# Kernel optimization log

Hardware: AMD Instinct MI355X
Metric: run time of the kernel (lower is better)

Reference implementation:

```python
import jax, jax.numpy as jnp
import numpy as np

N = 100000; C = 128; H = 8; G = C // 4
B = 2; Z = 40; Y = 996; X = 996
WIN = 12; NUM_WIN = 200; EPS = 1e-3


def _make_indices():
    rng = np.random.RandomState(0)
    total = B * Z * Y * X
    uk = np.unique(rng.randint(0, total, size=300000).astype(np.int64))[:N]
    b = uk // (Z * Y * X); r = uk % (Z * Y * X)
    z = r // (Y * X); r = r % (Y * X)
    y = r // X; x = r % X
    return b, z, y, x, uk


def _neighbors(b, z, y, x, keys, offsets):
    # submanifold conv: output only at active sites; lookup coord+offset in active set
    sk = np.sort(keys); order = np.argsort(keys)
    cols = []
    for dz, dy, dx in offsets:
        nz, ny, nx = z + dz, y + dy, x + dx
        valid = (nz >= 0) & (nz < Z) & (ny >= 0) & (ny < Y) & (nx >= 0) & (nx < X)
        cand = ((b * Z + nz) * Y + ny) * X + nx
        pos = np.searchsorted(sk, cand)
        posc = np.minimum(pos, N - 1)
        found = valid & (sk[posc] == cand)
        cols.append(np.where(found, order[posc], N))  # N = sentinel (zero row)
    return np.stack(cols, axis=1).astype(np.int32)


def setup_inputs() -> dict:
    b, z, y, x, keys = _make_indices()
    off_k = [(dz, dy, dx) for dz in (-1, 0, 1) for dy in (-1, 0, 1) for dx in (-1, 0, 1)]
    off_h = [(0, 0, d) for d in range(-6, 7)]  # kernel (1,1,13) along x
    off_w = [(0, d, 0) for d in range(-6, 7)]  # kernel (1,13,1) along y
    nbr_k = _neighbors(b, z, y, x, keys, off_k)
    nbr_h = _neighbors(b, z, y, x, keys, off_h)
    nbr_w = _neighbors(b, z, y, x, keys, off_w)
    coords = np.stack([y, x], axis=0)
    wis = []
    for d in range(2):
        wkey = b * 1000 + coords[d] // WIN
        _, inv = np.unique(wkey, return_inverse=True)
        wis.append(inv)
    win_inds = np.stack(wis, 0).astype(np.int32)

    ks = jax.random.split(jax.random.key(0), 20)
    s = 0.05
    return dict(
        feats=jax.random.normal(ks[0], (N, C), jnp.float32),
        win_inds=jnp.asarray(win_inds),
        nbr_k=jnp.asarray(nbr_k), nbr_h=jnp.asarray(nbr_h), nbr_w=jnp.asarray(nbr_w),
        bn_g=jnp.ones((2, C)) + s * jax.random.normal(ks[1], (2, C)),
        bn_b=s * jax.random.normal(ks[2], (2, C)),
        Wqkv=s * jax.random.normal(ks[3], (2, C, 3 * C)),
        Wproj=s * jax.random.normal(ks[4], (2, C, C)),
        bproj=s * jax.random.normal(ks[5], (2, C)),
        bn1_g=jnp.ones((2, C)) + s * jax.random.normal(ks[6], (2, C)),
        bn1_b=s * jax.random.normal(ks[7], (2, C)),
        Wk=s * jax.random.normal(ks[8], (2, 27, G, G)),
        Wh=s * jax.random.normal(ks[9], (2, 13, G, G)),
        Ww=s * jax.random.normal(ks[10], (2, 13, G, G)),
        bn2_g=jnp.ones((2, C)) + s * jax.random.normal(ks[11], (2, C)),
        bn2_b=s * jax.random.normal(ks[12], (2, C)),
        fc1_W=s * jax.random.normal(ks[13], (2, C, 2 * C)),
        fc1_b=s * jax.random.normal(ks[14], (2, 2 * C)),
        fc2_W=s * jax.random.normal(ks[15], (2, 2 * C, C)),
        fc2_b=s * jax.random.normal(ks[16], (2, C)),
    )


def _bn(x, g, b):
    # BatchNorm1d, training-mode batch statistics, eps=1e-3
    m = jnp.mean(x, 0)
    v = jnp.var(x, 0)
    return (x - m) * jax.lax.rsqrt(v + EPS) * g + b


def _attn(x, wi, Wqkv, Wp, bp):
    # windowed linear attention: per-window K^T V + normalization by sum(K)
    q, k, v = jnp.split(x @ Wqkv, 3, axis=1)
    q = jax.nn.relu(q).reshape(N, H, C // H)
    k = jax.nn.relu(k).reshape(N, H, C // H)
    v = v.reshape(N, H, C // H)
    kv = jax.ops.segment_sum(jnp.einsum('nhc,nhd->nhcd', k, v), wi, NUM_WIN)
    s = jax.ops.segment_sum(k, wi, NUM_WIN)
    y = jnp.einsum('nhc,nhcd->nhd', q, kv[wi])
    z = jnp.sum(s[wi] * q, -1, keepdims=True)
    y = (y / (z + EPS)).reshape(N, C)
    return y @ Wp + bp


def _subm(f, nbr, W):
    # submanifold sparse conv via precomputed neighbor map (sentinel row = zeros)
    fp = jnp.concatenate([f, jnp.zeros((1, f.shape[1]), f.dtype)], 0)
    return jnp.einsum('nkc,kcd->nd', fp[nbr], W)


def reference(feats, win_inds, nbr_k, nbr_h, nbr_w, bn_g, bn_b, Wqkv, Wproj, bproj,
              bn1_g, bn1_b, Wk, Wh, Ww, bn2_g, bn2_b, fc1_W, fc1_b, fc2_W, fc2_b):
    f = feats
    for d in range(2):  # directions
        x = _attn(_bn(f, bn_g[d], bn_b[d]), win_inds[d], Wqkv[d], Wproj[d], bproj[d])
        f = f + x
        # CWI_FFN_Layer_3D
        fb = _bn(f, bn1_g[d], bn1_b[d])
        f2 = jnp.concatenate([
            _subm(fb[:, :G], nbr_k, Wk[d]),
            _subm(fb[:, G:2 * G], nbr_h, Wh[d]),
            _subm(fb[:, 2 * G:3 * G], nbr_w, Ww[d]),
            fb[:, 3 * G:],
        ], axis=1)
        f = fb + f2
        h = _bn(f, bn2_g[d], bn2_b[d])
        f = f + (jax.nn.relu(h @ fc1_W[d] + fc1_b[d]) @ fc2_W[d] + fc2_b[d])
    return f
```

## Files before the change

### kernel.cpp

```cpp
#include <hip/hip_runtime.h>
#include <math.h>

#define NPTS 100000
#define CCH 128
#define NWIN 200
#define NBLK_STATS 512
#define NBLK_SORT 391
#define SEGSZ 128
#define NSEG_MAX 1024

#define BM 128
#define BN 128
#define BK 64

typedef __attribute__((ext_vector_type(8))) short bf16x8;
typedef __attribute__((ext_vector_type(4))) float f32x4;
typedef __attribute__((ext_vector_type(4))) unsigned short u16x4;

__device__ __forceinline__ unsigned short f2bf(float f) {
    union { float f; unsigned u; } x; x.f = f;
    unsigned r = x.u + 0x7fff + ((x.u >> 16) & 1);
    return (unsigned short)(r >> 16);
}
__device__ __forceinline__ float bf2f(unsigned short h) {
    union { unsigned u; float f; } x; x.u = ((unsigned)h) << 16;
    return x.f;
}

__global__ __launch_bounds__(256) void bn_partial(const float* __restrict__ F,
                                                  float* __restrict__ part) {
    int t = threadIdx.x;
    int b = blockIdx.x;
    int rg = t >> 5;
    int c4 = (t & 31) * 4;
    float s0=0.f,s1=0.f,s2=0.f,s3=0.f,q0=0.f,q1=0.f,q2=0.f,q3=0.f;
    for (int n = b * 8 + rg; n < NPTS; n += NBLK_STATS * 8) {
        float4 v = *reinterpret_cast<const float4*>(&F[(size_t)n * CCH + c4]);
        s0 += v.x; s1 += v.y; s2 += v.z; s3 += v.w;
        q0 += v.x*v.x; q1 += v.y*v.y; q2 += v.z*v.z; q3 += v.w*v.w;
    }
    __shared__ float red[8][256];
    red[rg][c4+0] = s0; red[rg][c4+1] = s1; red[rg][c4+2] = s2; red[rg][c4+3] = s3;
    red[rg][128+c4+0] = q0; red[rg][128+c4+1] = q1; red[rg][128+c4+2] = q2; red[rg][128+c4+3] = q3;
    __syncthreads();
    float a = 0.f;
#pragma unroll
    for (int g = 0; g < 8; g++) a += red[g][t];
    part[b * 256 + t] = a;
}

__global__ __launch_bounds__(256) void bnred_k(const float* __restrict__ part,
                                               float* __restrict__ part2) {
    int t = threadIdx.x;
    int i = blockIdx.x;
    float a = 0.f;
#pragma unroll 8
    for (int j = 0; j < 32; j++) a += part[(size_t)(i * 32 + j) * 256 + t];
    part2[i * 256 + t] = a;
}

__global__ void bn_finalize(const float* __restrict__ part2,
                            const float* __restrict__ g, const float* __restrict__ bb,
                            float* __restrict__ scale, float* __restrict__ shift) {
    int c = threadIdx.x;
    double s = 0.0, q = 0.0;
#pragma unroll
    for (int b = 0; b < 16; b++) {
        s += (double)part2[b * 256 + c];
        q += (double)part2[b * 256 + 128 + c];
    }
    double m = s / (double)NPTS;
    double var = q / (double)NPTS - m * m;
    double rstd = 1.0 / sqrt(var + 1e-3);
    float sc = (float)rstd * g[c];
    scale[c] = sc;
    shift[c] = bb[c] - (float)m * sc;
}

__global__ __launch_bounds__(128) void wprep(
    const float* __restrict__ W, int K, int N,
    const float* __restrict__ sc, const float* __restrict__ sh,
    const float* __restrict__ bias,
    unsigned short* __restrict__ WT, float* __restrict__ biasf)
{
    int n = blockIdx.x;
    int t = threadIdx.x;
    float part = 0.f;
    for (int k = t; k < K; k += 128) {
        float w = W[(size_t)k * N + n];
        float s = sc ? sc[k] * w : w;
        WT[(size_t)n * K + k] = f2bf(s);
        if (sh) part += sh[k] * w;
    }
    __shared__ float red[128];
    red[t] = part;
    __syncthreads();
    for (int o = 64; o > 0; o >>= 1) {
        if (t < o) red[t] += red[t + o];
        __syncthreads();
    }
    if (t == 0) biasf[n] = red[0] + (bias ? bias[n] : 0.f);
}

__global__ void wconv_prep_all(const float* __restrict__ Wk, const float* __restrict__ Wh,
                               const float* __restrict__ Ww, unsigned short* __restrict__ WB) {
    int i = blockIdx.x * 256 + threadIdx.x;
    if (i >= 53 * 1024) return;
    int tap = i >> 10; int rem = i & 1023; int dd = rem >> 5; int c = rem & 31;
    const float* src; int lt;
    if (tap < 27)      { src = Wk; lt = tap; }
    else if (tap < 40) { src = Wh; lt = tap - 27; }
    else               { src = Ww; lt = tap - 40; }
    WB[i] = f2bf(src[lt * 1024 + c * 32 + dd]);
}

template<int NT>
__global__ __launch_bounds__(256) void gemm_knt(
    const float* __restrict__ A, int lda,
    const unsigned short* __restrict__ WT, const float* __restrict__ biasf,
    unsigned short* __restrict__ Out, int ldo, int reluLim)
{
    __shared__ __align__(16) char smem[49664];
    unsigned short* As = (unsigned short*)smem;
    unsigned short* Bs = (unsigned short*)(smem + 32768);
    float* Ep = (float*)(smem + 32768);

    const int tid  = threadIdx.x;
    const int wave = tid >> 6;
    const int lane = tid & 63;
    const int bm = blockIdx.x * BM;
    const int lrow = lane & 15;
    const int lhk  = lane >> 4;

#pragma unroll
    for (int pass = 0; pass < 16; pass++) {
        int row = pass * 8 + (tid >> 5);
        int grow = bm + row;
        int c4 = (tid & 31) * 4;
        float4 v = make_float4(0.f, 0.f, 0.f, 0.f);
        if (grow < NPTS)
            v = *reinterpret_cast<const float4*>(&A[(size_t)grow * lda + c4]);
        u16x4 h4 = { f2bf(v.x), f2bf(v.y), f2bf(v.z), f2bf(v.w) };
        int half = c4 >> 6;
        int cw = c4 & 63;
        int sw = (cw >> 3) ^ (row & 7);
        *reinterpret_cast<u16x4*>(&As[row * 128 + half * 64 + sw * 8 + (cw & 7)]) = h4;
    }

    for (int nt = 0; nt < NT; nt++) {
        const int bn = nt * BN;
        f32x4 acc[2][8];
#pragma unroll
        for (int i = 0; i < 2; i++)
#pragma unroll
            for (int j = 0; j < 8; j++)
                acc[i][j] = (f32x4){0.f, 0.f, 0.f, 0.f};

#pragma unroll
        for (int h = 0; h < 2; h++) {
            __syncthreads();
#pragma unroll
            for (int pass = 0; pass < 4; pass++) {
                int n = pass * 32 + (tid >> 3);
                bf16x8 w = *reinterpret_cast<const bf16x8*>(
                    &WT[(size_t)(bn + n) * 128 + h * 64 + (tid & 7) * 8]);
                int sw = (tid & 7) ^ (n & 7);
                *reinterpret_cast<bf16x8*>(&Bs[n * 64 + sw * 8]) = w;
            }
            __syncthreads();
#pragma unroll
            for (int ks = 0; ks < 2; ks++) {
                bf16x8 af[2], bfr[8];
#pragma unroll
                for (int fi = 0; fi < 2; fi++) {
                    int row = wave * 32 + fi * 16 + lrow;
                    int sw = (ks * 4 + lhk) ^ (row & 7);
                    af[fi] = *reinterpret_cast<const bf16x8*>(&As[row * 128 + h * 64 + sw * 8]);
                }
#pragma unroll
                for (int fj = 0; fj < 8; fj++) {
                    int col = fj * 16 + lrow;
                    int sw = (ks * 4 + lhk) ^ (col & 7);
                    bfr[fj] = *reinterpret_cast<const bf16x8*>(&Bs[col * 64 + sw * 8]);
                }
#pragma unroll
                for (int fi = 0; fi < 2; fi++)
#pragma unroll
                    for (int fj = 0; fj < 8; fj++)
                        acc[fi][fj] = __builtin_amdgcn_mfma_f32_16x16x32_bf16(
                            af[fi], bfr[fj], acc[fi][fj], 0, 0, 0);
            }
        }
        __syncthreads();

#pragma unroll
        for (int ch = 0; ch < 4; ch++) {
            if (wave == ch) {
#pragma unroll
                for (int fi = 0; fi < 2; fi++)
#pragma unroll
                    for (int fj = 0; fj < 8; fj++) {
                        int r0 = fi * 16 + lhk * 4;
                        int col = fj * 16 + lrow;
#pragma unroll
                        for (int r = 0; r < 4; r++)
                            Ep[(r0 + r) * 132 + col] = acc[fi][fj][r];
                    }
            }
            __syncthreads();
#pragma unroll
            for (int pass = 0; pass < 4; pass++) {
                int idx = pass * 256 + tid;
                int r = idx >> 5;
                int c4 = (idx & 31) * 4;
                int rr = bm + ch * 32 + r;
                if (rr < NPTS) {
                    float4 v = *reinterpret_cast<const float4*>(&Ep[r * 132 + c4]);
                    float4 b = *reinterpret_cast<const float4*>(&biasf[bn + c4]);
                    v.x += b.x; v.y += b.y; v.z += b.z; v.w += b.w;
                    int col = bn + c4;
                    if (col + 0 < reluLim) v.x = fmaxf(v.x, 0.f);
                    if (col + 1 < reluLim) v.y = fmaxf(v.y, 0.f);
                    if (col + 2 < reluLim) v.z = fmaxf(v.z, 0.f);
                    if (col + 3 < reluLim) v.w = fmaxf(v.w, 0.f);
                    u16x4 hv = { f2bf(v.x), f2bf(v.y), f2bf(v.z), f2bf(v.w) };
                    *reinterpret_cast<u16x4*>(&Out[(size_t)rr * ldo + bn + c4]) = hv;
                }
            }
            __syncthreads();
        }
    }
}

template<int ABF, int OBF>
__global__ __launch_bounds__(256) void gemm_t(
    const void* __restrict__ Ap, int lda,
    const unsigned short* __restrict__ WT, const float* __restrict__ biasf,
    int K,
    void* __restrict__ Outp, int ldo,
    int reluLim, int addFlag)
{
    __shared__ __align__(16) char smem[34048];
    unsigned short* As = (unsigned short*)smem;
    unsigned short* Bs = As + BM * BK;
    float* Ep = (float*)smem;

    const int tid  = threadIdx.x;
    const int wave = tid >> 6;
    const int lane = tid & 63;
    const int bm = blockIdx.y * BM;
    const int bn = blockIdx.x * BN;

    f32x4 acc[2][8];
#pragma unroll
    for (int i = 0; i < 2; i++)
#pragma unroll
        for (int j = 0; j < 8; j++)
            acc[i][j] = (f32x4){0.f, 0.f, 0.f, 0.f};

    const int lrow = lane & 15;
    const int lhk  = lane >> 4;

    for (int kk = 0; kk < K; kk += BK) {
        if (ABF) {
            const unsigned short* Ab = (const unsigned short*)Ap;
#pragma unroll
            for (int pass = 0; pass < 4; pass++) {
                int row = pass * 32 + (tid >> 3);
                int grow = bm + row;
                bf16x8 w = (bf16x8){0,0,0,0,0,0,0,0};
                if (grow < NPTS)
                    w = *reinterpret_cast<const bf16x8*>(&Ab[(size_t)grow * lda + kk + (tid & 7) * 8]);
                int sw = (tid & 7) ^ (row & 7);
                *reinterpret_cast<bf16x8*>(&As[row * 64 + sw * 8]) = w;
            }
        } else {
            const float* Af = (const float*)Ap;
            const int arow_t = tid >> 4;
            const int acol   = (tid & 15) * 4;
#pragma unroll
            for (int pass = 0; pass < 8; pass++) {
                int row = pass * 16 + arow_t;
                int grow = bm + row;
                float4 v = make_float4(0.f, 0.f, 0.f, 0.f);
                if (grow < NPTS)
                    v = *reinterpret_cast<const float4*>(&Af[(size_t)grow * lda + kk + acol]);
                u16x4 h = { f2bf(v.x), f2bf(v.y), f2bf(v.z), f2bf(v.w) };
                int s = acol >> 3;
                int sw = s ^ (row & 7);
                *reinterpret_cast<u16x4*>(&As[row * 64 + sw * 8 + (acol & 7)]) = h;
            }
        }
#pragma unroll
        for (int pass = 0; pass < 4; pass++) {
            int n = pass * 32 + (tid >> 3);
            bf16x8 w = *reinterpret_cast<const bf16x8*>(&WT[(size_t)(bn + n) * K + kk + (tid & 7) * 8]);
            int sw = (tid & 7) ^ (n & 7);
            *reinterpret_cast<bf16x8*>(&Bs[n * 64 + sw * 8]) = w;
        }
        __syncthreads();

#pragma unroll
        for (int ks = 0; ks < 2; ks++) {
            bf16x8 af[2], bfr[8];
#pragma unroll
            for (int fi = 0; fi < 2; fi++) {
                int row = wave * 32 + fi * 16 + lrow;
                int sw = (ks * 4 + lhk) ^ (row & 7);
                af[fi] = *reinterpret_cast<const bf16x8*>(&As[row * 64 + sw * 8]);
            }
#pragma unroll
            for (int fj = 0; fj < 8; fj++) {
                int col = fj * 16 + lrow;
                int sw = (ks * 4 + lhk) ^ (col & 7);
                bfr[fj] = *reinterpret_cast<const bf16x8*>(&Bs[col * 64 + sw * 8]);
            }
#pragma unroll
            for (int fi = 0; fi < 2; fi++)
#pragma unroll
                for (int fj = 0; fj < 8; fj++)
                    acc[fi][fj] = __builtin_amdgcn_mfma_f32_16x16x32_bf16(
                        af[fi], bfr[fj], acc[fi][fj], 0, 0, 0);
        }
        __syncthreads();
    }

    for (int hh = 0; hh < 2; hh++) {
        if ((wave >> 1) == hh) {
#pragma unroll
            for (int fi = 0; fi < 2; fi++) {
                int row = (wave & 1) * 32 + fi * 16 + (lane >> 4) * 4;
#pragma unroll
                for (int fj = 0; fj < 8; fj++) {
                    int col = fj * 16 + (lane & 15);
#pragma unroll
                    for (int r = 0; r < 4; r++)
                        Ep[(row + r) * 132 + col] = acc[fi][fj][r];
                }
            }
        }
        __syncthreads();
#pragma unroll
        for (int pass = 0; pass < 8; pass++) {
            int idx = pass * 256 + tid;
            int r = idx >> 5;
            int c4 = (idx & 31) * 4;
            int rr = bm + hh * 64 + r;
            if (rr < NPTS) {
                float4 v = *reinterpret_cast<const float4*>(&Ep[r * 132 + c4]);
                float4 b = *reinterpret_cast<const float4*>(&biasf[bn + c4]);
                v.x += b.x; v.y += b.y; v.z += b.z; v.w += b.w;
                int col = bn + c4;
                if (col + 0 < reluLim) v.x = fmaxf(v.x, 0.f);
                if (col + 1 < reluLim) v.y = fmaxf(v.y, 0.f);
                if (col + 2 < reluLim) v.z = fmaxf(v.z, 0.f);
                if (col + 3 < reluLim) v.w = fmaxf(v.w, 0.f);
                if (OBF) {
                    unsigned short* o = (unsigned short*)Outp + (size_t)rr * ldo + bn + c4;
                    u16x4 hv = { f2bf(v.x), f2bf(v.y), f2bf(v.z), f2bf(v.w) };
                    *reinterpret_cast<u16x4*>(o) = hv;
                } else {
                    float* o = (float*)Outp + (size_t)rr * ldo + bn + c4;
                    if (addFlag) {
                        float4 ov = *reinterpret_cast<const float4*>(o);
                        v.x += ov.x; v.y += ov.y; v.z += ov.z; v.w += ov.w;
                    }
                    *reinterpret_cast<float4*>(o) = v;
                }
            }
        }
        __syncthreads();
    }
}

__global__ __launch_bounds__(256) void hist2_k(const int* __restrict__ wi,
                                               int* __restrict__ BH) {
    __shared__ int h[NWIN];
    int t = threadIdx.x;
    if (t < NWIN) h[t] = 0;
    __syncthreads();
    int n = blockIdx.x * 256 + t;
    if (n < NPTS) atomicAdd(&h[wi[n]], 1);
    __syncthreads();
    if (t < NWIN) BH[blockIdx.x * 256 + t] = h[t];
}

__global__ __launch_bounds__(256) void colscan2_k(const int* __restrict__ BH,
                                                  int* __restrict__ OFFB,
                                                  int* __restrict__ TOT) {
    int w = blockIdx.x;
    int t = threadIdx.x;
    __shared__ int s[512];
    int v0 = (t < NBLK_SORT) ? BH[t * 256 + w] : 0;
    int v1 = (t + 256 < NBLK_SORT) ? BH[(t + 256) * 256 + w] : 0;
    s[t] = v0; s[t + 256] = v1;
    __syncthreads();
#pragma unroll
    for (int off = 1; off < 512; off <<= 1) {
        int a0 = (t >= off) ? s[t - off] : 0;
        int a1 = (t + 256 >= off) ? s[t + 256 - off] : 0;
        __syncthreads();
        s[t] += a0;
        s[t + 256] += a1;
        __syncthreads();
    }
    if (t < NBLK_SORT) OFFB[t * 256 + w] = s[t] - v0;
    if (t + 256 < NBLK_SORT) OFFB[(t + 256) * 256 + w] = s[t + 256] - v1;
    if (t == 0) TOT[w] = s[NBLK_SORT - 1];
}

__global__ __launch_bounds__(256) void meta2_k(const int* __restrict__ TOT,
                                               int* __restrict__ OFFS,
                                               int* __restrict__ SEGW, int* __restrict__ SEGP0,
                                               int* __restrict__ SEGP1, int* __restrict__ SEGBASE) {
    __shared__ int offs[NWIN + 1];
    __shared__ int segc[NWIN];
    int t = threadIdx.x;
    if (t < NWIN) segc[t] = TOT[t];
    __syncthreads();
    if (t == 0) {
        int a = 0;
        for (int w = 0; w < NWIN; w++) { int c = segc[w]; offs[w] = a; a += c; }
        offs[NWIN] = a;
    }
    __syncthreads();
    if (t <= NWIN) OFFS[t] = offs[t];
    if (t < NWIN) segc[t] = (offs[t + 1] - offs[t] + SEGSZ - 1) / SEGSZ;
    __syncthreads();
    if (t == 0) {
        int a = 0;
        for (int i = 0; i < NWIN; i++) { int c = segc[i]; segc[i] = a; SEGBASE[i] = a; a += c; }
        SEGBASE[NWIN] = a;
    }
    __syncthreads();
    if (t < NWIN) {
        int b = segc[t];
        int p0 = offs[t], p1 = offs[t + 1];
        for (int p = p0; p < p1; p += SEGSZ) {
            SEGW[b] = t; SEGP0[b] = p; SEGP1[b] = min(p + SEGSZ, p1); b++;
        }
    }
}

__global__ __launch_bounds__(256) void scatter2_k(const int* __restrict__ wi,
                                                  const int* __restrict__ OFFS,
                                                  const int* __restrict__ OFFB,
                                                  int* __restrict__ list) {
    __shared__ int h[NWIN];
    int t = threadIdx.x;
    if (t < NWIN) h[t] = 0;
    __syncthreads();
    int n = blockIdx.x * 256 + t;
    if (n < NPTS) {
        int w = wi[n];
        int r = atomicAdd(&h[w], 1);
        list[OFFS[w] + OFFB[blockIdx.x * 256 + w] + r] = n;
    }
}

__global__ __launch_bounds__(256) void window_kv_seg(
    const unsigned short* __restrict__ R0bf,
    const int* __restrict__ list,
    const int* __restrict__ SEGP0, const int* __restrict__ SEGP1,
    const int* __restrict__ SEGBASE,
    float* __restrict__ PKV)
{
    int sid = blockIdx.x;
    if (sid >= SEGBASE[NWIN]) return;
    int t = threadIdx.x;
    int p0 = SEGP0[sid], p1 = SEGP1[sid];
    __shared__ float buf[8][256];
    float acc[8] = {0.f,0.f,0.f,0.f,0.f,0.f,0.f,0.f};
    float sa = 0.f;
    int f0 = t * 8;
    int h = f0 >> 8;
    int c = (f0 >> 4) & 15;
    int d0 = f0 & 15;
    const int sr = t >> 5;
    const int c8 = (t & 31) * 8;

    for (int g = p0; g < p1; g += 8) {
        int m = min(8, p1 - g);
        int nj[8];
#pragma unroll
        for (int j = 0; j < 8; j++)
            nj[j] = list[(g + j < p1) ? g + j : p1 - 1];
        __syncthreads();
        {
            const unsigned short* row = &R0bf[(size_t)nj[sr] * 384 + 128];
            bf16x8 hv = *reinterpret_cast<const bf16x8*>(&row[c8]);
            float4 lo = make_float4(bf2f((unsigned short)hv[0]), bf2f((unsigned short)hv[1]),
                                    bf2f((unsigned short)hv[2]), bf2f((unsigned short)hv[3]));
            float4 hi = make_float4(bf2f((unsigned short)hv[4]), bf2f((unsigned short)hv[5]),
                                    bf2f((unsigned short)hv[6]), bf2f((unsigned short)hv[7]));
            *reinterpret_cast<float4*>(&buf[sr][c8]) = lo;
            *reinterpret_cast<float4*>(&buf[sr][c8 + 4]) = hi;
        }
        __syncthreads();
#pragma unroll
        for (int j = 0; j < 8; j++) {
            if (j >= m) break;
            float kc = buf[j][h * 16 + c];
#pragma unroll
            for (int i = 0; i < 8; i++) acc[i] += kc * buf[j][128 + h * 16 + d0 + i];
            if (t < 128) sa += buf[j][t];
        }
    }
    float* out = &PKV[(size_t)sid * 2176];
#pragma unroll
    for (int i = 0; i < 8; i++) out[f0 + i] = acc[i];
    if (t < 128) out[2048 + t] = sa;
}

__global__ __launch_bounds__(256) void kv_reduce(
    const float* __restrict__ PKV, const int* __restrict__ SEGBASE,
    float* __restrict__ KV, float* __restrict__ SB)
{
    int w = blockIdx.x;
    int t = threadIdx.x;
    int s0 = SEGBASE[w], s1 = SEGBASE[w + 1];
    float a[8] = {0.f,0.f,0.f,0.f,0.f,0.f,0.f,0.f};
    float sb = 0.f;
    for (int s = s0; s < s1; s++) {
        const float* p = &PKV[(size_t)s * 2176];
#pragma unroll
        for (int i = 0; i < 8; i++) a[i] += p[t * 8 + i];
        if (t < 128) sb += p[2048 + t];
    }
#pragma unroll
    for (int i = 0; i < 8; i++) KV[w * 2048 + t * 8 + i] = a[i];
    if (t < 128) SB[w * 128 + t] = sb;
}

__global__ __launch_bounds__(256) void attn_y_seg(
    const unsigned short* __restrict__ R0bf,
    unsigned short* __restrict__ Ybf,
    const int* __restrict__ list,
    const int* __restrict__ SEGW, const int* __restrict__ SEGP0,
    const int* __restrict__ SEGP1, const int* __restrict__ SEGBASE,
    const float* __restrict__ KV, const float* __restrict__ SB)
{
    int sid = blockIdx.x;
    if (sid >= SEGBASE[NWIN]) return;
    int t = threadIdx.x;
    int w = SEGW[sid];
    int g  = t >> 5;
    int h  = (t >> 2) & 7;
    int d4 = (t & 3) * 4;

    float4 kvr[16];
    const float* kvb = &KV[w * 2048 + h * 256 + d4];
#pragma unroll
    for (int cc = 0; cc < 16; cc++)
        kvr[cc] = *reinterpret_cast<const float4*>(&kvb[cc * 16]);
    float sreg[16];
    const float* sb = &SB[w * 128 + h * 16];
#pragma unroll
    for (int cc = 0; cc < 16; cc++) sreg[cc] = sb[cc];

    int p0 = SEGP0[sid], p1 = SEGP1[sid];
    for (int p = p0 + g; p < p1; p += 8) {
        int n = list[p];
        const unsigned short* q = &R0bf[(size_t)n * 384 + h * 16];
        bf16x8 qa = *reinterpret_cast<const bf16x8*>(&q[0]);
        bf16x8 qb = *reinterpret_cast<const bf16x8*>(&q[8]);
        float qq[16];
#pragma unroll
        for (int i = 0; i < 8; i++) {
            qq[i] = bf2f((unsigned short)qa[i]);
            qq[8 + i] = bf2f((unsigned short)qb[i]);
        }
        float z = 0.f;
        float4 y = make_float4(0.f, 0.f, 0.f, 0.f);
#pragma unroll
        for (int cc = 0; cc < 16; cc++) {
            z += qq[cc] * sreg[cc];
            y.x += qq[cc] * kvr[cc].x;
            y.y += qq[cc] * kvr[cc].y;
            y.z += qq[cc] * kvr[cc].z;
            y.w += qq[cc] * kvr[cc].w;
        }
        float inv = 1.f / (z + 1e-3f);
        u16x4 o = { f2bf(y.x * inv), f2bf(y.y * inv), f2bf(y.z * inv), f2bf(y.w * inv) };
        *reinterpret_cast<u16x4*>(&Ybf[(size_t)n * 128 + h * 16 + d4]) = o;
    }
}

__global__ void bn_apply(float* F, unsigned short* __restrict__ FBbf,
                         const float* __restrict__ scale, const float* __restrict__ shift)
{
    int i = blockIdx.x * 256 + threadIdx.x;
    int n = i >> 5;
    int c4 = (i & 31) * 4;
    float4 v = *reinterpret_cast<const float4*>(&F[n * CCH + c4]);
    float4 o;
    o.x = v.x * scale[c4 + 0] + shift[c4 + 0];
    o.y = v.y * scale[c4 + 1] + shift[c4 + 1];
    o.z = v.z * scale[c4 + 2] + shift[c4 + 2];
    o.w = v.w * scale[c4 + 3] + shift[c4 + 3];
    u16x4 hv = { f2bf(o.x), f2bf(o.y), f2bf(o.z), f2bf(o.w) };
    *reinterpret_cast<u16x4*>(&FBbf[(size_t)n * 128 + c4]) = hv;
    if (c4 >= 96) {
        float4 t = make_float4(2.f * o.x, 2.f * o.y, 2.f * o.z, 2.f * o.w);
        *reinterpret_cast<float4*>(&F[n * CCH + c4]) = t;
    }
}

template<int KN>
__global__ __launch_bounds__(256) void conv_direct(
    const int* __restrict__ nbrA, const int* __restrict__ nbrB,
    const unsigned short* __restrict__ WBall, int wbBase,
    const unsigned short* __restrict__ FBbf,
    float* __restrict__ F, int offBase)
{
    const int which = blockIdx.y;
    const int* __restrict__ nbr = which ? nbrB : nbrA;
    const int off = offBase + which * 32;
    const unsigned short* __restrict__ WB = WBall + wbBase + which * KN * 1024;

    __shared__ __align__(16) float Ep[128 * 36];

    const int tid = threadIdx.x;
    const int wave = tid >> 6;
    const int lane = tid & 63;
    const int bm = blockIdx.x * 128;
    const int lrow = lane & 15;
    const int lk = lane >> 4;

    const int row0 = bm + wave * 32 + lrow;
    const int row1 = row0 + 16;

    f32x4 acc[2][2];
#pragma unroll
    for (int i = 0; i < 2; i++)
#pragma unroll
        for (int j = 0; j < 2; j++)
            acc[i][j] = (f32x4){0.f, 0.f, 0.f, 0.f};

    constexpr int CHK = (KN == 27) ? 9 : 13;
    for (int c0 = 0; c0 < KN; c0 += CHK) {
        int i0[CHK], i1[CHK];
#pragma unroll
        for (int j = 0; j < CHK; j++) {
            i0[j] = (row0 < NPTS) ? nbr[(size_t)row0 * KN + c0 + j] : NPTS;
            i1[j] = (row1 < NPTS) ? nbr[(size_t)row1 * KN + c0 + j] : NPTS;
        }
#pragma unroll
        for (int j = 0; j < CHK; j++) {
            int k = c0 + j;
            bf16x8 a0 = (bf16x8){0,0,0,0,0,0,0,0};
            bf16x8 a1 = (bf16x8){0,0,0,0,0,0,0,0};
            if (i0[j] < NPTS)
                a0 = *reinterpret_cast<const bf16x8*>(&FBbf[(size_t)i0[j] * 128 + off + lk * 8]);
            if (i1[j] < NPTS)
                a1 = *reinterpret_cast<const bf16x8*>(&FBbf[(size_t)i1[j] * 128 + off + lk * 8]);
            bf16x8 b0 = *reinterpret_cast<const bf16x8*>(&WB[k * 1024 + lrow * 32 + lk * 8]);
            bf16x8 b1 = *reinterpret_cast<const bf16x8*>(&WB[k * 1024 + (16 + lrow) * 32 + lk * 8]);
            acc[0][0] = __builtin_amdgcn_mfma_f32_16x16x32_bf16(a0, b0, acc[0][0], 0, 0, 0);
            acc[0][1] = __builtin_amdgcn_mfma_f32_16x16x32_bf16(a0, b1, acc[0][1], 0, 0, 0);
            acc[1][0] = __builtin_amdgcn_mfma_f32_16x16x32_bf16(a1, b0, acc[1][0], 0, 0, 0);
            acc[1][1] = __builtin_amdgcn_mfma_f32_16x16x32_bf16(a1, b1, acc[1][1], 0, 0, 0);
        }
    }

#pragma unroll
    for (int fi = 0; fi < 2; fi++)
#pragma unroll
        for (int fj = 0; fj < 2; fj++) {
            int r0 = wave * 32 + fi * 16 + lk * 4;
            int col = fj * 16 + lrow;
#pragma unroll
            for (int r = 0; r < 4; r++)
                Ep[(r0 + r) * 36 + col] = acc[fi][fj][r];
        }
    __syncthreads();
#pragma unroll
    for (int pass = 0; pass < 4; pass++) {
        int idx = pass * 256 + tid;
        int r = idx >> 3;
        int c4 = (idx & 7) * 4;
        int rr = bm + r;
        if (rr < NPTS) {
            float4 v = *reinterpret_cast<const float4*>(&Ep[r * 36 + c4]);
            u16x4 fbh = *reinterpret_cast<const u16x4*>(&FBbf[(size_t)rr * 128 + off + c4]);
            v.x += bf2f(fbh.x); v.y += bf2f(fbh.y);
            v.z += bf2f(fbh.z); v.w += bf2f(fbh.w);
            *reinterpret_cast<float4*>(&F[(size_t)rr * CCH + off + c4]) = v;
        }
    }
}

extern "C" void kernel_launch(void* const* d_in, const int* in_sizes, int n_in,
                              void* d_out, int out_size, void* d_ws, size_t ws_size,
                              hipStream_t stream)
{
    const float* feats   = (const float*)d_in[0];
    const int*   win_inds= (const int*)d_in[1];
    const int*   nbr_k   = (const int*)d_in[2];
    const int*   nbr_h   = (const int*)d_in[3];
    const int*   nbr_w   = (const int*)d_in[4];
    const float* bn_g    = (const float*)d_in[5];
    const float* bn_b    = (const float*)d_in[6];
    const float* Wqkv    = (const float*)d_in[7];
    const float* Wproj   = (const float*)d_in[8];
    const float* bproj   = (const float*)d_in[9];
    const float* bn1_g   = (const float*)d_in[10];
    const float* bn1_b   = (const float*)d_in[11];
    const float* Wk      = (const float*)d_in[12];
    const float* Wh      = (const float*)d_in[13];
    const float* Ww      = (const float*)d_in[14];
    const float* bn2_g   = (const float*)d_in[15];
    const float* bn2_b   = (const float*)d_in[16];
    const float* fc1_W   = (const float*)d_in[17];
    const float* fc1_b   = (const float*)d_in[18];
    const float* fc2_W   = (const float*)d_in[19];
    const float* fc2_b   = (const float*)d_in[20];

    float* F  = (float*)d_out;
    float* KV = (float*)d_ws;
    float* SB = KV + NWIN * 2048;
    float* ST = SB + NWIN * 128;
    float* PART = ST + 768;
    float* PART2 = PART + NBLK_STATS * 256;
    float* PKV = PART2 + 16 * 256;
    int* OFFS = (int*)(PKV + (size_t)NSEG_MAX * 2176);
    int* TOT  = OFFS + 256;
    int* LIST = TOT + 256;
    int* BH   = LIST + 100096;
    int* OFFB = BH + NBLK_SORT * 256;
    int* SEGW = OFFB + NBLK_SORT * 256;
    int* SEGP0= SEGW + NSEG_MAX;
    int* SEGP1= SEGP0 + NSEG_MAX;
    int* SEGBASE = SEGP1 + NSEG_MAX;
    unsigned short* WQKVT = (unsigned short*)(SEGBASE + 256);
    unsigned short* WPROJT = WQKVT + 384 * 128;
    unsigned short* WFC1T  = WPROJT + 128 * 128;
    unsigned short* WFC2T  = WFC1T + 256 * 128;
    float* BQKV  = (float*)(WFC2T + 128 * 256);
    float* BPROJ = BQKV + 384;
    float* BFC1  = BPROJ + 128;
    float* BFC2  = BFC1 + 256;
    unsigned short* R0bf = (unsigned short*)(BFC2 + 128);
    unsigned short* Hbf  = R0bf;
    unsigned short* Ybf  = R0bf + (size_t)NPTS * 384;
    unsigned short* FBbf = Ybf + (size_t)NPTS * 128;
    unsigned short* WBall= FBbf + (size_t)NPTS * 128;

    hipMemcpyAsync(F, feats, (size_t)NPTS * CCH * sizeof(float),
                   hipMemcpyDeviceToDevice, stream);

    dim3 g1(1, 782);
    dim3 gc13(782, 2);

    for (int d = 0; d < 2; d++) {
        const int* wi = win_inds + (size_t)d * NPTS;
        float* SC0 = ST, *SH0 = ST + 128, *SC1 = ST + 256, *SH1 = ST + 384,
             * SC2 = ST + 512, *SH2 = ST + 640;

        bn_partial<<<NBLK_STATS, 256, 0, stream>>>(F, PART);
        bnred_k<<<16, 256, 0, stream>>>(PART, PART2);
        bn_finalize<<<1, 128, 0, stream>>>(PART2, bn_g + d * CCH, bn_b + d * CCH, SC0, SH0);
        wprep<<<384, 128, 0, stream>>>(Wqkv + (size_t)d * CCH * 384, 128, 384,
                                       SC0, SH0, nullptr, WQKVT, BQKV);
        wprep<<<128, 128, 0, stream>>>(Wproj + (size_t)d * CCH * CCH, 128, 128,
                                       nullptr, nullptr, bproj + d * CCH, WPROJT, BPROJ);
        wconv_prep_all<<<212, 256, 0, stream>>>(Wk + (size_t)d * 27 * 1024,
                                                Wh + (size_t)d * 13 * 1024,
                                                Ww + (size_t)d * 13 * 1024, WBall);

        gemm_knt<3><<<782, 256, 0, stream>>>(F, CCH, WQKVT, BQKV, R0bf, 384, 256);

        hist2_k<<<NBLK_SORT, 256, 0, stream>>>(wi, BH);
        colscan2_k<<<NWIN, 256, 0, stream>>>(BH, OFFB, TOT);
        meta2_k<<<1, 256, 0, stream>>>(TOT, OFFS, SEGW, SEGP0, SEGP1, SEGBASE);
        scatter2_k<<<NBLK_SORT, 256, 0, stream>>>(wi, OFFS, OFFB, LIST);

        window_kv_seg<<<NSEG_MAX, 256, 0, stream>>>(R0bf, LIST, SEGP0, SEGP1, SEGBASE, PKV);
        kv_reduce<<<NWIN, 256, 0, stream>>>(PKV, SEGBASE, KV, SB);

        attn_y_seg<<<NSEG_MAX, 256, 0, stream>>>(R0bf, Ybf, LIST, SEGW, SEGP0, SEGP1,
                                                 SEGBASE, KV, SB);

        gemm_t<1,0><<<g1, 256, 0, stream>>>(Ybf, 128, WPROJT, BPROJ, 128,
                                            F, CCH, 0, 1);

        bn_partial<<<NBLK_STATS, 256, 0, stream>>>(F, PART);
        bnred_k<<<16, 256, 0, stream>>>(PART, PART2);
        bn_finalize<<<1, 128, 0, stream>>>(PART2, bn1_g + d * CCH, bn1_b + d * CCH, SC1, SH1);
        bn_apply<<<12500, 256, 0, stream>>>(F, FBbf, SC1, SH1);

        conv_direct<27><<<782, 256, 0, stream>>>(nbr_k, nbr_k, WBall, 0, FBbf, F, 0);
        conv_direct<13><<<gc13, 256, 0, stream>>>(nbr_h, nbr_w, WBall, 27 * 1024, FBbf, F, 32);

        bn_partial<<<NBLK_STATS, 256, 0, stream>>>(F, PART);
        bnred_k<<<16, 256, 0, stream>>>(PART, PART2);
        bn_finalize<<<1, 128, 0, stream>>>(PART2, bn2_g + d * CCH, bn2_b + d * CCH, SC2, SH2);
        wprep<<<256, 128, 0, stream>>>(fc1_W + (size_t)d * CCH * 256, 128, 256,
                                       SC2, SH2, fc1_b + d * 256, WFC1T, BFC1);
        wprep<<<128, 128, 0, stream>>>(fc2_W + (size_t)d * 256 * CCH, 256, 128,
                                       nullptr, nullptr, fc2_b + d * CCH, WFC2T, BFC2);

        gemm_knt<2><<<782, 256, 0, stream>>>(F, CCH, WFC1T, BFC1, Hbf, 256, 256);
        gemm_t<1,0><<<g1, 256, 0, stream>>>(Hbf, 256, WFC2T, BFC2, 256,
                                            F, CCH, 0, 1);
    }
}
```

Before: 724.7 us.

## Fuse BatchNorm statistics into residual GEMM epilogues and initial copy

The BN sum and sum-of-squares partials are now computed inside the residual-add GEMM epilogue (new gemm_res) and inside a copy kernel that replaces the initial memcpy. This removes the separate bn_partial passes that re-read the full feature tensor after the projection and FC2 GEMMs. bnred_k now takes a variable partial-block count. The bf16-output GEMM epilogue also writes straight from registers with scalar stores instead of staging through LDS, which removes barriers but gives less coalesced writes.

```diff
diff --git a/kernel.cpp b/kernel.cpp
--- a/kernel.cpp
+++ b/kernel.cpp
@@ -5,6 +5,7 @@
 #define CCH 128
 #define NWIN 200
 #define NBLK_STATS 512
+#define NBLK_GEMM 782
 #define NBLK_SORT 391
 #define SEGSZ 128
 #define NSEG_MAX 1024
@@ -25,6 +26,30 @@
 __device__ __forceinline__ float bf2f(unsigned short h) {
     union { unsigned u; float f; } x; x.u = ((unsigned)h) << 16;
     return x.f;
+}
+
+__global__ __launch_bounds__(256) void copy_stats(const float* __restrict__ src,
+                                                  float* __restrict__ F,
+                                                  float* __restrict__ part) {
+    int t = threadIdx.x;
+    int b = blockIdx.x;
+    int rg = t >> 5;
+    int c4 = (t & 31) * 4;
+    float s0=0.f,s1=0.f,s2=0.f,s3=0.f,q0=0.f,q1=0.f,q2=0.f,q3=0.f;
+    for (int n = b * 8 + rg; n < NPTS; n += NBLK_STATS * 8) {
+        float4 v = *reinterpret_cast<const float4*>(&src[(size_t)n * CCH + c4]);
+        *reinterpret_cast<float4*>(&F[(size_t)n * CCH + c4]) = v;
+        s0 += v.x; s1 += v.y; s2 += v.z; s3 += v.w;
+        q0 += v.x*v.x; q1 += v.y*v.y; q2 += v.z*v.z; q3 += v.w*v.w;
+    }
+    __shared__ float red[8][256];
+    red[rg][c4+0] = s0; red[rg][c4+1] = s1; red[rg][c4+2] = s2; red[rg][c4+3] = s3;
+    red[rg][128+c4+0] = q0; red[rg][128+c4+1] = q1; red[rg][128+c4+2] = q2; red[rg][128+c4+3] = q3;
+    __syncthreads();
+    float a = 0.f;
+#pragma unroll
+    for (int g = 0; g < 8; g++) a += red[g][t];
+    part[b * 256 + t] = a;
 }
 
 __global__ __launch_bounds__(256) void bn_partial(const float* __restrict__ F,
@@ -50,12 +75,15 @@
 }
 
 __global__ __launch_bounds__(256) void bnred_k(const float* __restrict__ part,
-                                               float* __restrict__ part2) {
+                                               float* __restrict__ part2, int nblk) {
     int t = threadIdx.x;
     int i = blockIdx.x;
+    int chunk = (nblk + 15) >> 4;
     float a = 0.f;
-#pragma unroll 8
-    for (int j = 0; j < 32; j++) a += part[(size_t)(i * 32 + j) * 256 + t];
+    for (int j = 0; j < chunk; j++) {
+        int idx = i * chunk + j;
+        if (idx < nblk) a += part[(size_t)idx * 256 + t];
+    }
     part2[i * 256 + t] = a;
 }
 
@@ -120,10 +148,9 @@
     const unsigned short* __restrict__ WT, const float* __restrict__ biasf,
     unsigned short* __restrict__ Out, int ldo, int reluLim)
 {
-    __shared__ __align__(16) char smem[49664];
+    __shared__ __align__(16) char smem[49152];
     unsigned short* As = (unsigned short*)smem;
     unsigned short* Bs = (unsigned short*)(smem + 32768);
-    float* Ep = (float*)(smem + 32768);
 
     const int tid  = threadIdx.x;
     const int wave = tid >> 6;
@@ -191,54 +218,35 @@
                             af[fi], bfr[fj], acc[fi][fj], 0, 0, 0);
             }
         }
-        __syncthreads();
-
-#pragma unroll
-        for (int ch = 0; ch < 4; ch++) {
-            if (wave == ch) {
-#pragma unroll
-                for (int fi = 0; fi < 2; fi++)
-#pragma unroll
-                    for (int fj = 0; fj < 8; fj++) {
-                        int r0 = fi * 16 + lhk * 4;
-                        int col = fj * 16 + lrow;
-#pragma unroll
-                        for (int r = 0; r < 4; r++)
-                            Ep[(r0 + r) * 132 + col] = acc[fi][fj][r];
+
+#pragma unroll
+        for (int fi = 0; fi < 2; fi++) {
+            int rbase = bm + wave * 32 + fi * 16 + lhk * 4;
+#pragma unroll
+            for (int fj = 0; fj < 8; fj++) {
+                int col = bn + fj * 16 + lrow;
+                float bv = biasf[col];
+                bool rl = col < reluLim;
+#pragma unroll
+                for (int r = 0; r < 4; r++) {
+                    int rr = rbase + r;
+                    if (rr < NPTS) {
+                        float v = acc[fi][fj][r] + bv;
+                        if (rl) v = fmaxf(v, 0.f);
+                        Out[(size_t)rr * ldo + col] = f2bf(v);
                     }
-            }
-            __syncthreads();
-#pragma unroll
-            for (int pass = 0; pass < 4; pass++) {
-                int idx = pass * 256 + tid;
-                int r = idx >> 5;
-                int c4 = (idx & 31) * 4;
-                int rr = bm + ch * 32 + r;
-                if (rr < NPTS) {
-                    float4 v = *reinterpret_cast<const float4*>(&Ep[r * 132 + c4]);
-                    float4 b = *reinterpret_cast<const float4*>(&biasf[bn + c4]);
-                    v.x += b.x; v.y += b.y; v.z += b.z; v.w += b.w;
-                    int col = bn + c4;
-                    if (col + 0 < reluLim) v.x = fmaxf(v.x, 0.f);
-                    if (col + 1 < reluLim) v.y = fmaxf(v.y, 0.f);
-                    if (col + 2 < reluLim) v.z = fmaxf(v.z, 0.f);
-                    if (col + 3 < reluLim) v.w = fmaxf(v.w, 0.f);
-                    u16x4 hv = { f2bf(v.x), f2bf(v.y), f2bf(v.z), f2bf(v.w) };
-                    *reinterpret_cast<u16x4*>(&Out[(size_t)rr * ldo + bn + c4]) = hv;
                 }
             }
-            __syncthreads();
-        }
-    }
-}
-
-template<int ABF, int OBF>
-__global__ __launch_bounds__(256) void gemm_t(
-    const void* __restrict__ Ap, int lda,
+        }
+    }
+}
+
+__global__ __launch_bounds__(256) void gemm_res(
+    const unsigned short* __restrict__ Ab, int lda,
     const unsigned short* __restrict__ WT, const float* __restrict__ biasf,
     int K,
-    void* __restrict__ Outp, int ldo,
-    int reluLim, int addFlag)
+    float* __restrict__ Outp, int ldo,
+    float* __restrict__ partOut)
 {
     __shared__ __align__(16) char smem[34048];
     unsigned short* As = (unsigned short*)smem;
@@ -249,7 +257,7 @@
     const int wave = tid >> 6;
     const int lane = tid & 63;
     const int bm = blockIdx.y * BM;
-    const int bn = blockIdx.x * BN;
+    const int bn = 0;
 
     f32x4 acc[2][8];
 #pragma unroll
@@ -262,34 +270,15 @@
     const int lhk  = lane >> 4;
 
     for (int kk = 0; kk < K; kk += BK) {
-        if (ABF) {
-            const unsigned short* Ab = (const unsigned short*)Ap;
-#pragma unroll
-            for (int pass = 0; pass < 4; pass++) {
-                int row = pass * 32 + (tid >> 3);
-                int grow = bm + row;
-                bf16x8 w = (bf16x8){0,0,0,0,0,0,0,0};
-                if (grow < NPTS)
-                    w = *reinterpret_cast<const bf16x8*>(&Ab[(size_t)grow * lda + kk + (tid & 7) * 8]);
-                int sw = (tid & 7) ^ (row & 7);
-                *reinterpret_cast<bf16x8*>(&As[row * 64 + sw * 8]) = w;
-            }
-        } else {
-            const float* Af = (const float*)Ap;
-            const int arow_t = tid >> 4;
-            const int acol   = (tid & 15) * 4;
-#pragma unroll
-            for (int pass = 0; pass < 8; pass++) {
-                int row = pass * 16 + arow_t;
-                int grow = bm + row;
-                float4 v = make_float4(0.f, 0.f, 0.f, 0.f);
-                if (grow < NPTS)
-                    v = *reinterpret_cast<const float4*>(&Af[(size_t)grow * lda + kk + acol]);
-                u16x4 h = { f2bf(v.x), f2bf(v.y), f2bf(v.z), f2bf(v.w) };
-                int s = acol >> 3;
-                int sw = s ^ (row & 7);
-                *reinterpret_cast<u16x4*>(&As[row * 64 + sw * 8 + (acol & 7)]) = h;
-            }
+#pragma unroll
+        for (int pass = 0; pass < 4; pass++) {
+            int row = pass * 32 + (tid >> 3);
+            int grow = bm + row;
+            bf16x8 w = (bf16x8){0,0,0,0,0,0,0,0};
+            if (grow < NPTS)
+                w = *reinterpret_cast<const bf16x8*>(&Ab[(size_t)grow * lda + kk + (tid & 7) * 8]);
+            int sw = (tid & 7) ^ (row & 7);
+            *reinterpret_cast<bf16x8*>(&As[row * 64 + sw * 8]) = w;
         }
 #pragma unroll
         for (int pass = 0; pass < 4; pass++) {
@@ -325,6 +314,7 @@
         __syncthreads();
     }
 
+    float s0=0.f,s1=0.f,s2=0.f,s3=0.f,q0=0.f,q1=0.f,q2=0.f,q3=0.f;
     for (int hh = 0; hh < 2; hh++) {
         if ((wave >> 1) == hh) {
 #pragma unroll
@@ -348,28 +338,31 @@
             int rr = bm + hh * 64 + r;
             if (rr < NPTS) {
                 float4 v = *reinterpret_cast<const float4*>(&Ep[r * 132 + c4]);
-                float4 b = *reinterpret_cast<const float4*>(&biasf[bn + c4]);
+                float4 b = *reinterpret_cast<const float4*>(&biasf[c4]);
                 v.x += b.x; v.y += b.y; v.z += b.z; v.w += b.w;
-                int col = bn + c4;
-                if (col + 0 < reluLim) v.x = fmaxf(v.x, 0.f);
-                if (col + 1 < reluLim) v.y = fmaxf(v.y, 0.f);
-                if (col + 2 < reluLim) v.z = fmaxf(v.z, 0.f);
-                if (col + 3 < reluLim) v.w = fmaxf(v.w, 0.f);
-                if (OBF) {
-                    unsigned short* o = (unsigned short*)Outp + (size_t)rr * ldo + bn + c4;
-                    u16x4 hv = { f2bf(v.x), f2bf(v.y), f2bf(v.z), f2bf(v.w) };
-                    *reinterpret_cast<u16x4*>(o) = hv;
-                } else {
-                    float* o = (float*)Outp + (size_t)rr * ldo + bn + c4;
-                    if (addFlag) {
-                        float4 ov = *reinterpret_cast<const float4*>(o);
-                        v.x += ov.x; v.y += ov.y; v.z += ov.z; v.w += ov.w;
-                    }
-                    *reinterpret_cast<float4*>(o) = v;
-                }
+                float* o = &Outp[(size_t)rr * ldo + c4];
+                float4 ov = *reinterpret_cast<const float4*>(o);
+                v.x += ov.x; v.y += ov.y; v.z += ov.z; v.w += ov.w;
+                *reinterpret_cast<float4*>(o) = v;
+                s0 += v.x; s1 += v.y; s2 += v.z; s3 += v.w;
+                q0 += v.x*v.x; q1 += v.y*v.y; q2 += v.z*v.z; q3 += v.w*v.w;
             }
         }
         __syncthreads();
+    }
+    if (partOut) {
+        float* red = (float*)smem;
+        int rg = tid >> 5;
+        int c4 = (tid & 31) * 4;
+        red[rg * 256 + c4 + 0] = s0; red[rg * 256 + c4 + 1] = s1;
+        red[rg * 256 + c4 + 2] = s2; red[rg * 256 + c4 + 3] = s3;
+        red[rg * 256 + 128 + c4 + 0] = q0; red[rg * 256 + 128 + c4 + 1] = q1;
+        red[rg * 256 + 128 + c4 + 2] = q2; red[rg * 256 + 128 + c4 + 3] = q3;
+        __syncthreads();
+        float a = 0.f;
+#pragma unroll
+        for (int g = 0; g < 8; g++) a += red[g * 256 + tid];
+        partOut[(size_t)blockIdx.y * 256 + tid] = a;
     }
 }
 
@@ -721,7 +714,7 @@
     float* SB = KV + NWIN * 2048;
     float* ST = SB + NWIN * 128;
     float* PART = ST + 768;
-    float* PART2 = PART + NBLK_STATS * 256;
+    float* PART2 = PART + (size_t)NBLK_GEMM * 256;
     float* PKV = PART2 + 16 * 256;
     int* OFFS = (int*)(PKV + (size_t)NSEG_MAX * 2176);
     int* TOT  = OFFS + 256;
@@ -746,19 +739,17 @@
     unsigned short* FBbf = Ybf + (size_t)NPTS * 128;
     unsigned short* WBall= FBbf + (size_t)NPTS * 128;
 
-    hipMemcpyAsync(F, feats, (size_t)NPTS * CCH * sizeof(float),
-                   hipMemcpyDeviceToDevice, stream);
-
-    dim3 g1(1, 782);
-    dim3 gc13(782, 2);
+    copy_stats<<<NBLK_STATS, 256, 0, stream>>>(feats, F, PART);
+
+    dim3 g1(1, NBLK_GEMM);
+    dim3 gc13(NBLK_GEMM, 2);
 
     for (int d = 0; d < 2; d++) {
         const int* wi = win_inds + (size_t)d * NPTS;
         float* SC0 = ST, *SH0 = ST + 128, *SC1 = ST + 256, *SH1 = ST + 384,
              * SC2 = ST + 512, *SH2 = ST + 640;
 
-        bn_partial<<<NBLK_STATS, 256, 0, stream>>>(F, PART);
-        bnred_k<<<16, 256, 0, stream>>>(PART, PART2);
+        bnred_k<<<16, 256, 0, stream>>>(PART, PART2, d == 0 ? NBLK_STATS : NBLK_GEMM);
         bn_finalize<<<1, 128, 0, stream>>>(PART2, bn_g + d * CCH, bn_b + d * CCH, SC0, SH0);
         wprep<<<384, 128, 0, stream>>>(Wqkv + (size_t)d * CCH * 384, 128, 384,
                                        SC0, SH0, nullptr, WQKVT, BQKV);
@@ -768,7 +759,7 @@
                                                 Wh + (size_t)d * 13 * 1024,
                                                 Ww + (size_t)d * 13 * 1024, WBall);
 
-        gemm_knt<3><<<782, 256, 0, stream>>>(F, CCH, WQKVT, BQKV, R0bf, 384, 256);
+        gemm_knt<3><<<NBLK_GEMM, 256, 0, stream>>>(F, CCH, WQKVT, BQKV, R0bf, 384, 256);
 
         hist2_k<<<NBLK_SORT, 256, 0, stream>>>(wi, BH);
         colscan2_k<<<NWIN, 256, 0, stream>>>(BH, OFFB, TOT);
@@ -781,27 +772,24 @@
         attn_y_seg<<<NSEG_MAX, 256, 0, stream>>>(R0bf, Ybf, LIST, SEGW, SEGP0, SEGP1,
                                                  SEGBASE, KV, SB);
 
-        gemm_t<1,0><<<g1, 256, 0, stream>>>(Ybf, 128, WPROJT, BPROJ, 128,
-                                            F, CCH, 0, 1);
-
-        bn_partial<<<NBLK_STATS, 256, 0, stream>>>(F, PART);
-        bnred_k<<<16, 256, 0, stream>>>(PART, PART2);
+        gemm_res<<<g1, 256, 0, stream>>>(Ybf, 128, WPROJT, BPROJ, 128, F, CCH, PART);
+
+        bnred_k<<<16, 256, 0, stream>>>(PART, PART2, NBLK_GEMM);
         bn_finalize<<<1, 128, 0, stream>>>(PART2, bn1_g + d * CCH, bn1_b + d * CCH, SC1, SH1);
         bn_apply<<<12500, 256, 0, stream>>>(F, FBbf, SC1, SH1);
 
-        conv_direct<27><<<782, 256, 0, stream>>>(nbr_k, nbr_k, WBall, 0, FBbf, F, 0);
+        conv_direct<27><<<NBLK_GEMM, 256, 0, stream>>>(nbr_k, nbr_k, WBall, 0, FBbf, F, 0);
         conv_direct<13><<<gc13, 256, 0, stream>>>(nbr_h, nbr_w, WBall, 27 * 1024, FBbf, F, 32);
 
         bn_partial<<<NBLK_STATS, 256, 0, stream>>>(F, PART);
-        bnred_k<<<16, 256, 0, stream>>>(PART, PART2);
+        bnred_k<<<16, 256, 0, stream>>>(PART, PART2, NBLK_STATS);
         bn_finalize<<<1, 128, 0, stream>>>(PART2, bn2_g + d * CCH, bn2_b + d * CCH, SC2, SH2);
         wprep<<<256, 128, 0, stream>>>(fc1_W + (size_t)d * CCH * 256, 128, 256,
                                        SC2, SH2, fc1_b + d * 256, WFC1T, BFC1);
         wprep<<<128, 128, 0, stream>>>(fc2_W + (size_t)d * 256 * CCH, 256, 128,
                                        nullptr, nullptr, fc2_b + d * CCH, WFC2T, BFC2);
 
-        gemm_knt<2><<<782, 256, 0, stream>>>(F, CCH, WFC1T, BFC1, Hbf, 256, 256);
-        gemm_t<1,0><<<g1, 256, 0, stream>>>(Hbf, 256, WFC2T, BFC2, 256,
-                                            F, CCH, 0, 1);
-    }
-}
+        gemm_knt<2><<<NBLK_GEMM, 256, 0, stream>>>(F, CCH, WFC1T, BFC1, Hbf, 256, 256);
+        gemm_res<<<g1, 256, 0, stream>>>(Hbf, 256, WFC2T, BFC2, 256, F, CCH, PART);
+    }
+}
```

Result: slower. 755.6 us (+4.3%).
